# Optimization experiments

Hardware: AMD Instinct MI355X
Metric: run time of the kernel (lower is better)

Reference implementation:

```python
import jax, jax.numpy as jnp
import numpy as np

D_MODEL = 2048
N_HEADS = 32
N_KV_HEADS = 8
HEAD_DIM = D_MODEL // N_HEADS  # 64
THETA = 10000.0
BATCH = 2
SEQ = 2048


def _rope_tables(seq_len, head_dim, theta):
    idx = jnp.arange(0, head_dim, 2, dtype=jnp.float32)
    inv_freq = 1.0 / (theta ** (idx / head_dim))
    pos = jnp.arange(seq_len, dtype=jnp.float32)
    angles = pos[:, None] * inv_freq[None, :]  # (S, head_dim/2)
    return jnp.cos(angles), jnp.sin(angles)


def _apply_rope(x, cos, sin):
    # x: (B, H, S, Dh); cos/sin: (S, Dh/2)
    c = cos[None, None, :, :]
    s = sin[None, None, :, :]
    x_even = x[..., 0::2]
    x_odd = x[..., 1::2]
    out_even = x_even * c - x_odd * s
    out_odd = x_even * s + x_odd * c
    # interleave back: stack on last axis and reshape
    return jnp.stack([out_even, out_odd], axis=-1).reshape(x.shape)


def setup_inputs() -> dict:
    key = jax.random.key(0)
    kx, kq, kk, kv, ko = jax.random.split(key, 5)
    std_sq = (2.0 / (D_MODEL + D_MODEL)) ** 0.5
    std_kv = (2.0 / (D_MODEL + N_KV_HEADS * HEAD_DIM)) ** 0.5
    return {
        "x": jax.random.normal(kx, (BATCH, SEQ, D_MODEL), dtype=jnp.float32),
        "Wq": jax.random.normal(kq, (D_MODEL, D_MODEL), dtype=jnp.float32) * std_sq,
        "Wk": jax.random.normal(kk, (N_KV_HEADS * HEAD_DIM, D_MODEL), dtype=jnp.float32) * std_kv,
        "Wv": jax.random.normal(kv, (N_KV_HEADS * HEAD_DIM, D_MODEL), dtype=jnp.float32) * std_kv,
        "Wo": jax.random.normal(ko, (D_MODEL, D_MODEL), dtype=jnp.float32) * std_sq,
    }


def reference(x, Wq, Wk, Wv, Wo):
    B, S, D = x.shape
    groups = N_HEADS // N_KV_HEADS
    cos, sin = _rope_tables(S, HEAD_DIM, THETA)

    q = (x @ Wq.T).reshape(B, S, N_HEADS, HEAD_DIM).transpose(0, 2, 1, 3)
    k = (x @ Wk.T).reshape(B, S, N_KV_HEADS, HEAD_DIM).transpose(0, 2, 1, 3)
    v = (x @ Wv.T).reshape(B, S, N_KV_HEADS, HEAD_DIM).transpose(0, 2, 1, 3)

    q = _apply_rope(q, cos, sin)
    k = _apply_rope(k, cos, sin)

    # GQA: repeat kv heads (repeat_interleave along head dim)
    k = jnp.repeat(k, groups, axis=1)  # (B, H, S, Dh)
    v = jnp.repeat(v, groups, axis=1)

    scale = 1.0 / jnp.sqrt(jnp.float32(HEAD_DIM))
    scores = jnp.einsum('bhqd,bhkd->bhqk', q, k) * scale
    causal = jnp.tril(jnp.ones((S, S), dtype=bool))
    scores = jnp.where(causal[None, None, :, :], scores, -jnp.inf)
    attn = jax.nn.softmax(scores, axis=-1)
    out = jnp.einsum('bhqk,bhkd->bhqd', attn, v)
    out = out.transpose(0, 2, 1, 3).reshape(B, S, D)
    return out @ Wo.T
```

## Files before the change

### kernel.cpp

```cpp
#include <hip/hip_runtime.h>
#include <math.h>

#define BATCHN 2
#define SEQ 2048
#define DMODEL 2048
#define NH 32
#define NKV 8
#define HDIM 64
#define KVD 512
#define ROWS 4096

typedef __bf16 bf16x8 __attribute__((ext_vector_type(8)));
typedef float f32x4 __attribute__((ext_vector_type(4)));
typedef unsigned short u16x8 __attribute__((ext_vector_type(8)));

#define MFMA(a, b, c) __builtin_amdgcn_mfma_f32_16x16x32_bf16(a, b, c, 0, 0, 0)

__device__ __forceinline__ unsigned short f2bf(float f) {
  union { float f; unsigned u; } v; v.f = f;
  unsigned u = v.u;
  u += 0x7fffu + ((u >> 16) & 1u);
  return (unsigned short)(u >> 16);
}

__device__ __forceinline__ unsigned cvtpk(float a, float b) {
  unsigned r;
  asm("v_cvt_pk_bf16_f32 %0, %1, %2" : "=v"(r) : "v"(a), "v"(b));
  return r;
}
__device__ __forceinline__ void pl32(unsigned& a, unsigned& b) {
  asm("v_permlane32_swap_b32 %0, %1" : "+v"(a), "+v"(b));
}
__device__ __forceinline__ void pl16(unsigned& a, unsigned& b) {
  asm("v_permlane16_swap_b32 %0, %1" : "+v"(a), "+v"(b));
}
__device__ __forceinline__ float exp2v(float x) {
  float r;
  asm("v_exp_f32 %0, %1" : "=v"(r) : "v"(x));
  return r;
}

__device__ __forceinline__ void gload16(const void* g, void* l) {
  __builtin_amdgcn_global_load_lds((const __attribute__((address_space(1))) unsigned int*)g,
                                   (__attribute__((address_space(3))) unsigned int*)l, 16, 0, 0);
}

#define FENCE() asm volatile("" ::: "memory")
#define BARRIER() do { FENCE(); __builtin_amdgcn_s_barrier(); FENCE(); } while (0)
#define LGKM0() asm volatile("s_waitcnt lgkmcnt(0)" ::: "memory")
#define VMCNT(n) asm volatile("s_waitcnt vmcnt(" #n ")" ::: "memory")

__global__ __launch_bounds__(256) void conv_all(const float* __restrict__ x,
                                                const float* __restrict__ Wq,
                                                const float* __restrict__ Wk,
                                                const float* __restrict__ Wv,
                                                const float* __restrict__ Wo,
                                                unsigned short* __restrict__ xb,
                                                unsigned short* __restrict__ Wqb,
                                                unsigned short* __restrict__ Wkb,
                                                unsigned short* __restrict__ Wvb,
                                                unsigned short* __restrict__ Wob,
                                                float* __restrict__ ct,
                                                float* __restrict__ st) {
  int i = blockIdx.x * 256 + threadIdx.x;
  const float* in;
  unsigned short* out;
  int off;
  if (i < 2097152)      { in = x;  out = xb;  off = i; }
  else if (i < 3145728) { in = Wq; out = Wqb; off = i - 2097152; }
  else if (i < 3407872) { in = Wk; out = Wkb; off = i - 3145728; }
  else if (i < 3670016) { in = Wv; out = Wvb; off = i - 3407872; }
  else if (i < 4718592) { in = Wo; out = Wob; off = i - 3670016; }
  else {
    int t = i - 4718592;
    int s = t >> 5, f = t & 31;
    float inv = __expf(-(float)f * (9.210340371976184f / 32.0f));
    float ang = (float)s * inv;
    ct[t] = cosf(ang);
    st[t] = sinf(ang);
    return;
  }
  float4 v = ((const float4*)in)[off];
  ushort4 o;
  o.x = f2bf(v.x); o.y = f2bf(v.y); o.z = f2bf(v.z); o.w = f2bf(v.w);
  ((ushort4*)out)[off] = o;
}

__global__ __launch_bounds__(512, 4) void gemm_qkv8p(const unsigned short* __restrict__ A,
                                                     const unsigned short* __restrict__ Bq,
                                                     const unsigned short* __restrict__ Bk,
                                                     const unsigned short* __restrict__ Bv,
                                                     unsigned short* __restrict__ Qo,
                                                     unsigned short* __restrict__ Ko,
                                                     unsigned short* __restrict__ Vt,
                                                     const float* __restrict__ ct,
                                                     const float* __restrict__ st) {
  __shared__ __align__(16) unsigned short Als[2][128 * 64];
  __shared__ __align__(16) unsigned short Bls[2][128 * 64];
  const int tid = threadIdx.x;
  const int lane = tid & 63, wv = tid >> 6;
  const int wm = wv >> 2, wn = wv & 3;
  const int g = lane >> 4, r15 = lane & 15;
  const int wgid = (blockIdx.x & 7) * 96 + (blockIdx.x >> 3);
  const int bm = wgid / 24, bn = wgid % 24;
  const int row0 = bm << 7;
  const unsigned short* Bp;
  unsigned short* Outb = nullptr;
  int col0, ldo = 0, rope = 0, qsc = 0, isv = 0;
  if (bn < 16)      { Bp = Bq; Outb = Qo; col0 = bn << 7;        ldo = DMODEL; rope = 1; qsc = 1; }
  else if (bn < 20) { Bp = Bk; Outb = Ko; col0 = (bn - 16) << 7; ldo = KVD;    rope = 1; }
  else              { Bp = Bv; col0 = (bn - 20) << 7; isv = 1; }
  const int srow = (wv << 3) + ((lane >> 3) & 7);
  const int scol = (((lane & 7) ^ ((lane >> 3) & 7)) << 3);
  const unsigned short* gA = A + (size_t)(row0 + srow) * DMODEL + scol;
  const unsigned short* gB = Bp + (size_t)(col0 + srow) * DMODEL + scol;
  const int ldsoff = (wv << 9);

  f32x4 acc[4][2];
#pragma unroll
  for (int i = 0; i < 4; ++i) { acc[i][0] = (f32x4){0,0,0,0}; acc[i][1] = (f32x4){0,0,0,0}; }

#define STAGE_A(buf, t, j) gload16(gA + (size_t)((t) * 64) + (size_t)((j) * 64) * DMODEL, \
                                   &Als[buf][(j) * 4096 + ldsoff])
#define STAGE_B(buf, t, j) gload16(gB + (size_t)((t) * 64) + (size_t)((j) * 64) * DMODEL, \
                                   &Bls[buf][(j) * 4096 + ldsoff])
#define RD_A(buf, mf, kk) (*(const bf16x8*)&Als[buf][((wm << 6) + ((mf) << 4) + r15) * 64 + \
                            ((((kk) << 2) + g) ^ (r15 & 7)) * 8])
#define RD_B(buf, nf, kk) (*(const bf16x8*)&Bls[buf][((wn << 5) + ((nf) << 4) + r15) * 64 + \
                            ((((kk) << 2) + g) ^ (r15 & 7)) * 8])

  STAGE_A(0, 0, 0); STAGE_A(0, 0, 1); STAGE_B(0, 0, 0); STAGE_B(0, 0, 1);
  STAGE_A(1, 1, 0); STAGE_A(1, 1, 1); STAGE_B(1, 1, 0); STAGE_B(1, 1, 1);
  VMCNT(4);
  BARRIER();

  const int NT = DMODEL / 64;
  for (int t = 0; t < NT; ++t) {
    const int cur = t & 1;
    bf16x8 bfr[2][2];
#pragma unroll
    for (int nf = 0; nf < 2; ++nf)
#pragma unroll
      for (int kk = 0; kk < 2; ++kk) bfr[nf][kk] = RD_B(cur, nf, kk);
    bf16x8 a00 = RD_A(cur, 0, 0), a01 = RD_A(cur, 0, 1);
    bf16x8 a10 = RD_A(cur, 1, 0), a11 = RD_A(cur, 1, 1);
    if (t >= 1 && t + 1 < NT) { STAGE_A(cur ^ 1, t + 1, 0); STAGE_A(cur ^ 1, t + 1, 1); }
    BARRIER();
    __builtin_amdgcn_s_setprio(1);
#pragma unroll
    for (int nf = 0; nf < 2; ++nf) {
      acc[0][nf] = MFMA(a00, bfr[nf][0], acc[0][nf]);
      acc[0][nf] = MFMA(a01, bfr[nf][1], acc[0][nf]);
      acc[1][nf] = MFMA(a10, bfr[nf][0], acc[1][nf]);
      acc[1][nf] = MFMA(a11, bfr[nf][1], acc[1][nf]);
    }
    __builtin_amdgcn_s_setprio(0);
    BARRIER();
    bf16x8 a20 = RD_A(cur, 2, 0), a21 = RD_A(cur, 2, 1);
    bf16x8 a30 = RD_A(cur, 3, 0), a31 = RD_A(cur, 3, 1);
    if (t + 2 < NT) { STAGE_B(cur, t + 2, 0); STAGE_B(cur, t + 2, 1); }
    BARRIER();
    __builtin_amdgcn_s_setprio(1);
#pragma unroll
    for (int nf = 0; nf < 2; ++nf) {
      acc[2][nf] = MFMA(a20, bfr[nf][0], acc[2][nf]);
      acc[2][nf] = MFMA(a21, bfr[nf][1], acc[2][nf]);
      acc[3][nf] = MFMA(a30, bfr[nf][0], acc[3][nf]);
      acc[3][nf] = MFMA(a31, bfr[nf][1], acc[3][nf]);
    }
    __builtin_amdgcn_s_setprio(0);
    if (t < NT - 1) {
      if (t == NT - 2) VMCNT(0);
      else             VMCNT(2);
    }
    BARRIER();
  }

  if (isv) {
#pragma unroll
    for (int mf = 0; mf < 4; ++mf) {
      const int m0 = row0 + (wm << 6) + (mf << 4) + (g << 2);
      const int b = m0 >> 11, s0 = m0 & (SEQ - 1);
#pragma unroll
      for (int nf = 0; nf < 2; ++nf) {
        const int nv = col0 + (wn << 5) + (nf << 4) + r15;
        ushort4 o;
        o.x = f2bf(acc[mf][nf][0]);
        o.y = f2bf(acc[mf][nf][1]);
        o.z = f2bf(acc[mf][nf][2]);
        o.w = f2bf(acc[mf][nf][3]);
        *(ushort4*)(Vt + ((size_t)(b * NKV * HDIM + nv)) * SEQ + s0) = o;
      }
    }
  } else {
    const float QS = 0.18033688011112042f;
#pragma unroll
    for (int mf = 0; mf < 4; ++mf) {
#pragma unroll
      for (int rr = 0; rr < 4; ++rr) {
        const int m = row0 + (wm << 6) + (mf << 4) + (g << 2) + rr;
        const float* ctr = ct + ((m & (SEQ - 1)) << 5);
        const float* str = st + ((m & (SEQ - 1)) << 5);
#pragma unroll
        for (int nf = 0; nf < 2; ++nf) {
          const int n = col0 + (wn << 5) + (nf << 4) + r15;
          float v = acc[mf][nf][rr];
          float p = __shfl_xor(v, 1);
          if (rope) {
            int fi = (n & 63) >> 1;
            float c = ctr[fi], sn = str[fi];
            v = (lane & 1) ? (p * sn + v * c) : (v * c - p * sn);
          }
          if (qsc) v *= QS;
          Outb[(size_t)m * ldo + n] = f2bf(v);
        }
      }
    }
  }
#undef STAGE_A
#undef STAGE_B
#undef RD_A
#undef RD_B
}

__global__ __launch_bounds__(512) void gemm_out128(const unsigned short* __restrict__ A,
                                                   const unsigned short* __restrict__ B,
                                                   float* __restrict__ C) {
  __shared__ __align__(16) unsigned short Als[3][8192];
  __shared__ __align__(16) unsigned short Bls[3][2][8192];
  const int tid = threadIdx.x, lane = tid & 63, wv = tid >> 6;
  const int wm = wv >> 2, wn = wv & 3;
  const int g = lane >> 4, r15 = lane & 15;
  const int wgid = (blockIdx.x & 7) * 32 + (blockIdx.x >> 3);
  const int bm = wgid >> 3, bn = wgid & 7;
  const int row0 = bm << 7, col0 = bn << 8;
  const int srl = tid >> 3;
  const int sgc = ((tid & 7) ^ (srl & 7)) << 3;
  const unsigned short* gA = A + (size_t)(row0 + srl) * DMODEL + sgc;
  const unsigned short* gB = B + (size_t)(col0 + srl) * DMODEL + sgc;

  f32x4 acc[4][4];
#pragma unroll
  for (int i = 0; i < 4; ++i)
#pragma unroll
    for (int jj = 0; jj < 4; ++jj) acc[i][jj] = (f32x4){0.f, 0.f, 0.f, 0.f};

#define STG_A1(buf, kt) do { \
    gload16(gA + (size_t)(kt) * 64, &Als[buf][(wv << 9)]); \
    gload16(gA + (size_t)64 * DMODEL + (size_t)(kt) * 64, &Als[buf][4096 + (wv << 9)]); } while (0)
#define STG_B1(buf, h, kt) do { \
    gload16(gB + (size_t)((h) * 128) * DMODEL + (kt) * 64, &Bls[buf][h][(wv << 9)]); \
    gload16(gB + (size_t)((h) * 128 + 64) * DMODEL + (kt) * 64, &Bls[buf][h][4096 + (wv << 9)]); } while (0)
#define RA1(buf, mf, kk) (*(const bf16x8*)&Als[buf][((wm << 6) + (mf) * 16 + r15) * 64 + \
                           (((((kk) << 2) + g) ^ (r15 & 7)) << 3)])
#define RB1(buf, nf, kk) (*(const bf16x8*)&Bls[buf][wn >> 1][((wn & 1) * 64 + (nf) * 16 + r15) * 64 + \
                           (((((kk) << 2) + g) ^ (r15 & 7)) << 3)])

  STG_B1(0, 0, 0); STG_B1(0, 1, 0); STG_A1(0, 0);
  STG_B1(1, 0, 1); STG_B1(1, 1, 1); STG_A1(1, 1);
  VMCNT(6);
  BARRIER();

  const int NT = DMODEL / 64;
  for (int t = 0; t < NT; ++t) {
    const int cur = t % 3;
    const int stg = (t + 2) % 3;
    bf16x8 a[4][2], b0[2][2];
#pragma unroll
    for (int mf = 0; mf < 4; ++mf) { a[mf][0] = RA1(cur, mf, 0); a[mf][1] = RA1(cur, mf, 1); }
#pragma unroll
    for (int nf = 0; nf < 2; ++nf) { b0[nf][0] = RB1(cur, nf, 0); b0[nf][1] = RB1(cur, nf, 1); }
    if (t + 2 < NT) { STG_B1(stg, 0, t + 2); STG_B1(stg, 1, t + 2); }
    BARRIER();
    __builtin_amdgcn_s_setprio(1);
#pragma unroll
    for (int mf = 0; mf < 4; ++mf)
#pragma unroll
      for (int nf = 0; nf < 2; ++nf) {
        acc[mf][nf] = MFMA(a[mf][0], b0[nf][0], acc[mf][nf]);
        acc[mf][nf] = MFMA(a[mf][1], b0[nf][1], acc[mf][nf]);
      }
    __builtin_amdgcn_s_setprio(0);
    BARRIER();
    bf16x8 b2[2][2];
#pragma unroll
    for (int nf = 0; nf < 2; ++nf) { b2[nf][0] = RB1(cur, 2 + nf, 0); b2[nf][1] = RB1(cur, 2 + nf, 1); }
    if (t + 2 < NT) STG_A1(stg, t + 2);
    BARRIER();
    __builtin_amdgcn_s_setprio(1);
#pragma unroll
    for (int mf = 0; mf < 4; ++mf)
#pragma unroll
      for (int nf = 0; nf < 2; ++nf) {
        acc[mf][2 + nf] = MFMA(a[mf][0], b2[nf][0], acc[mf][2 + nf]);
        acc[mf][2 + nf] = MFMA(a[mf][1], b2[nf][1], acc[mf][2 + nf]);
      }
    __builtin_amdgcn_s_setprio(0);
    if (t + 2 < NT) { VMCNT(6); }
    else if (t + 2 == NT) { VMCNT(0); }
    BARRIER();
  }
#undef STG_A1
#undef STG_B1
#undef RA1
#undef RB1

#pragma unroll
  for (int mf = 0; mf < 4; ++mf)
#pragma unroll
    for (int rr = 0; rr < 4; ++rr) {
      const int m = row0 + (wm << 6) + (mf) * 16 + (g << 2) + rr;
#pragma unroll
      for (int nf = 0; nf < 4; ++nf)
        C[(size_t)m * DMODEL + col0 + (wn << 6) + (nf << 4) + r15] = acc[mf][nf][rr];
    }
}

__global__ __launch_bounds__(512) void attn_fwd(const unsigned short* __restrict__ Q,
                                                const unsigned short* __restrict__ K,
                                                const unsigned short* __restrict__ Vt,
                                                unsigned short* __restrict__ O) {
  __shared__ __align__(16) unsigned short Kls[2][64 * 64];
  __shared__ __align__(16) unsigned short Vls[2][64 * 64];
  const int bid = blockIdx.x;
  const int xcd = bid & 7;
  const int within = bid >> 3;
  const int grp = xcd * 2 + (within >> 5);
  const int w32 = within & 31;
  const int j = w32 & 7;
  const int hsub = w32 >> 3;
  const int b = grp >> 3, kvh = grp & 7;
  const int h = kvh * 4 + hsub;
  const int wave = threadIdx.x >> 6, lane = threadIdx.x & 63;
  const int g = lane >> 4, r15 = lane & 15;
  const int sr = lane >> 3;
  const int sc = (((lane & 7) << 4) ^ (sr << 4)) >> 1;
  const unsigned short* kbase = K + (size_t)b * SEQ * KVD + kvh * HDIM;
  const unsigned short* vbase = Vt + (size_t)((b * NKV + kvh) * HDIM) * SEQ;

  union { u16x8 s; bf16x8 v; } one8;
#pragma unroll
  for (int z = 0; z < 8; ++z) one8.s[z] = 0x3F80;

  auto STAGE = [&](int bi, int kbv) {
    const int r = wave * 8;
    gload16(kbase + (size_t)(kbv + r + sr) * KVD + sc, &Kls[bi][r * 64]);
    gload16(vbase + (size_t)(r + sr) * SEQ + kbv + sc, &Vls[bi][r * 64]);
  };

#pragma unroll 1
  for (int sel = 0; sel < 2; ++sel) {
    const int qt = sel ? (15 - j) : j;
    const int qrow0 = qt * 128 + wave * 16;
    const unsigned short* qp = Q + (size_t)(b * SEQ + qrow0 + r15) * DMODEL + h * HDIM;
    bf16x8 q0 = *(const bf16x8*)(qp + g * 8);
    bf16x8 q1 = *(const bf16x8*)(qp + 32 + g * 8);
    f32x4 oacc[4] = {};
    f32x4 lacc = {};
    const int kend = (qt + 1) * 128;
    __syncthreads();
    STAGE(0, 0);
    int buf = 0;
    for (int kb = 0; kb < kend; kb += 64) {
      __syncthreads();
      if (kb + 64 < kend) STAGE(buf ^ 1, kb + 64);
      const char* Kc = (const char*)&Kls[buf][0];
      const char* Vc = (const char*)&Vls[buf][0];
      f32x4 s[4];
      __builtin_amdgcn_s_setprio(1);
#pragma unroll
      for (int f = 0; f < 4; ++f) {
        const int r = f * 16 + r15;
        const int sw = (r & 7) << 4;
        bf16x8 k0 = *(const bf16x8*)(Kc + r * 128 + ((g * 16) ^ sw));
        bf16x8 k1 = *(const bf16x8*)(Kc + r * 128 + ((64 + g * 16) ^ sw));
        f32x4 z = {};
        s[f] = MFMA(k1, q1, MFMA(k0, q0, z));
      }
      __builtin_amdgcn_s_setprio(0);
      if (kb + 64 > qrow0) {
        const int q = qrow0 + r15;
#pragma unroll
        for (int f = 0; f < 4; ++f)
#pragma unroll
          for (int rr = 0; rr < 4; ++rr)
            if (kb + f * 16 + g * 4 + rr > q) s[f][rr] = -1e30f;
      }
#pragma unroll
      for (int f = 0; f < 4; ++f)
#pragma unroll
        for (int rr = 0; rr < 4; ++rr) s[f][rr] = exp2v(s[f][rr]);
      bf16x8 p1, p2;
      {
        union { bf16x8 v; unsigned u[4]; } P1, P2;
        unsigned a0 = cvtpk(s[0][0], s[0][1]), b0 = cvtpk(s[1][0], s[1][1]);
        pl32(a0, b0); pl16(a0, b0);
        unsigned a1 = cvtpk(s[0][2], s[0][3]), b1 = cvtpk(s[1][2], s[1][3]);
        pl32(a1, b1); pl16(a1, b1);
        P1.u[0] = a0; P1.u[1] = a1; P1.u[2] = b0; P1.u[3] = b1;
        unsigned a2 = cvtpk(s[2][0], s[2][1]), b2 = cvtpk(s[3][0], s[3][1]);
        pl32(a2, b2); pl16(a2, b2);
        unsigned a3 = cvtpk(s[2][2], s[2][3]), b3 = cvtpk(s[3][2], s[3][3]);
        pl32(a3, b3); pl16(a3, b3);
        P2.u[0] = a2; P2.u[1] = a3; P2.u[2] = b2; P2.u[3] = b3;
        p1 = P1.v; p2 = P2.v;
      }
      lacc = MFMA(p2, one8.v, MFMA(p1, one8.v, lacc));
      __builtin_amdgcn_s_setprio(1);
#pragma unroll
      for (int dc = 0; dc < 4; ++dc) {
        const int r = dc * 16 + r15;
        const int sw = (r & 7) << 4;
        bf16x8 v0 = *(const bf16x8*)(Vc + r * 128 + ((g * 16) ^ sw));
        bf16x8 v1 = *(const bf16x8*)(Vc + r * 128 + ((64 + g * 16) ^ sw));
        oacc[dc] = MFMA(p2, v1, MFMA(p1, v0, oacc[dc]));
      }
      __builtin_amdgcn_s_setprio(0);
      buf ^= 1;
    }
    float rls[4];
#pragma unroll
    for (int rr = 0; rr < 4; ++rr) rls[rr] = 1.0f / lacc[rr];
    unsigned short* optr = O + (size_t)(b * SEQ + qrow0) * DMODEL + h * HDIM;
#pragma unroll
    for (int dc = 0; dc < 4; ++dc)
#pragma unroll
      for (int rr = 0; rr < 4; ++rr)
        optr[(size_t)(g * 4 + rr) * DMODEL + dc * 16 + r15] = f2bf(oacc[dc][rr] * rls[rr]);
  }
}

extern "C" void kernel_launch(void* const* d_in, const int* in_sizes, int n_in,
                              void* d_out, int out_size, void* d_ws, size_t ws_size,
                              hipStream_t stream) {
  const float* x  = (const float*)d_in[0];
  const float* Wq = (const float*)d_in[1];
  const float* Wk = (const float*)d_in[2];
  const float* Wv = (const float*)d_in[3];
  const float* Wo = (const float*)d_in[4];

  char* ws = (char*)d_ws;
  unsigned short* xb  = (unsigned short*)(ws);
  unsigned short* Wqb = (unsigned short*)(ws + (16u << 20));
  unsigned short* Wkb = (unsigned short*)(ws + (24u << 20));
  unsigned short* Wvb = (unsigned short*)(ws + (26u << 20));
  unsigned short* Wob = (unsigned short*)(ws + (28u << 20));
  unsigned short* Qb  = (unsigned short*)(ws + (36u << 20));
  unsigned short* Kb  = (unsigned short*)(ws + (52u << 20));
  unsigned short* Vtb = (unsigned short*)(ws + (60u << 20));
  unsigned short* AO  = (unsigned short*)(ws + (64u << 20));
  float* ct = (float*)(ws + (80u << 20));
  float* st = (float*)(ws + (81u << 20));

  conv_all<<<18688, 256, 0, stream>>>(x, Wq, Wk, Wv, Wo, xb, Wqb, Wkb, Wvb, Wob, ct, st);

  gemm_qkv8p<<<768, 512, 0, stream>>>(xb, Wqb, Wkb, Wvb, Qb, Kb, Vtb, ct, st);

  attn_fwd<<<512, 512, 0, stream>>>(Qb, Kb, Vtb, AO);

  gemm_out128<<<256, 512, 0, stream>>>(AO, Wob, (float*)d_out);
}
```

Measured before the change: 185.4 us.

## Widen QKV GEMM tiles to 128x384 with three B panels per block

The fused QKV projection now has each block compute a 128-row by 384-column tile made of three 128-column weight panels. The grid shrinks from 768 to 256 blocks, exactly one wave on the device's CUs. Each A fragment loaded from LDS feeds three times as many MFMAs, and A traffic from global memory drops threefold. A is triple-buffered and B double-buffered in LDS. The cost is more accumulator registers (launch bounds cut to 2 waves per SIMD), a larger LDS footprint, and a block remap that places blocks sharing rows on the same XCD.

Result: faster. 161.9 us (-12.7%).

```diff
diff --git a/kernel.cpp b/kernel.cpp
--- a/kernel.cpp
+++ b/kernel.cpp
@@ -47,7 +47,6 @@
 
 #define FENCE() asm volatile("" ::: "memory")
 #define BARRIER() do { FENCE(); __builtin_amdgcn_s_barrier(); FENCE(); } while (0)
-#define LGKM0() asm volatile("s_waitcnt lgkmcnt(0)" ::: "memory")
 #define VMCNT(n) asm volatile("s_waitcnt vmcnt(" #n ")" ::: "memory")
 
 __global__ __launch_bounds__(256) void conv_all(const float* __restrict__ x,
@@ -86,141 +85,166 @@
   ((ushort4*)out)[off] = o;
 }
 
-__global__ __launch_bounds__(512, 4) void gemm_qkv8p(const unsigned short* __restrict__ A,
-                                                     const unsigned short* __restrict__ Bq,
-                                                     const unsigned short* __restrict__ Bk,
-                                                     const unsigned short* __restrict__ Bv,
-                                                     unsigned short* __restrict__ Qo,
-                                                     unsigned short* __restrict__ Ko,
-                                                     unsigned short* __restrict__ Vt,
-                                                     const float* __restrict__ ct,
-                                                     const float* __restrict__ st) {
-  __shared__ __align__(16) unsigned short Als[2][128 * 64];
-  __shared__ __align__(16) unsigned short Bls[2][128 * 64];
-  const int tid = threadIdx.x;
-  const int lane = tid & 63, wv = tid >> 6;
+__global__ __launch_bounds__(512, 2) void gemm_qkv384(const unsigned short* __restrict__ A,
+                                                      const unsigned short* __restrict__ Bq,
+                                                      const unsigned short* __restrict__ Bk,
+                                                      const unsigned short* __restrict__ Bv,
+                                                      unsigned short* __restrict__ Qo,
+                                                      unsigned short* __restrict__ Ko,
+                                                      unsigned short* __restrict__ Vt,
+                                                      const float* __restrict__ ct,
+                                                      const float* __restrict__ st) {
+  __shared__ __align__(16) unsigned short Als[3][8192];
+  __shared__ __align__(16) unsigned short Bls[3][2][8192];
+  const int tid = threadIdx.x, lane = tid & 63, wv = tid >> 6;
   const int wm = wv >> 2, wn = wv & 3;
   const int g = lane >> 4, r15 = lane & 15;
-  const int wgid = (blockIdx.x & 7) * 96 + (blockIdx.x >> 3);
-  const int bm = wgid / 24, bn = wgid % 24;
+  const int c = blockIdx.x & 7, i = blockIdx.x >> 3;
+  const int bm = (c >> 1) * 8 + (i & 7);
+  const int grp = (c & 1) * 4 + (i >> 3);
   const int row0 = bm << 7;
-  const unsigned short* Bp;
-  unsigned short* Outb = nullptr;
-  int col0, ldo = 0, rope = 0, qsc = 0, isv = 0;
-  if (bn < 16)      { Bp = Bq; Outb = Qo; col0 = bn << 7;        ldo = DMODEL; rope = 1; qsc = 1; }
-  else if (bn < 20) { Bp = Bk; Outb = Ko; col0 = (bn - 16) << 7; ldo = KVD;    rope = 1; }
-  else              { Bp = Bv; col0 = (bn - 20) << 7; isv = 1; }
-  const int srow = (wv << 3) + ((lane >> 3) & 7);
-  const int scol = (((lane & 7) ^ ((lane >> 3) & 7)) << 3);
+  const unsigned short* Bpan[3];
+  int bnp[3];
+#pragma unroll
+  for (int bk = 0; bk < 3; ++bk) {
+    int p = grp * 3 + bk;
+    bnp[bk] = p;
+    Bpan[bk] = (p < 16) ? Bq + (size_t)(p << 7) * DMODEL
+             : (p < 20) ? Bk + (size_t)((p - 16) << 7) * DMODEL
+                        : Bv + (size_t)((p - 20) << 7) * DMODEL;
+  }
+  const int srow = tid >> 3;
+  const int scol = (((tid & 7) ^ ((tid >> 3) & 7)) << 3);
   const unsigned short* gA = A + (size_t)(row0 + srow) * DMODEL + scol;
-  const unsigned short* gB = Bp + (size_t)(col0 + srow) * DMODEL + scol;
-  const int ldsoff = (wv << 9);
-
-  f32x4 acc[4][2];
-#pragma unroll
-  for (int i = 0; i < 4; ++i) { acc[i][0] = (f32x4){0,0,0,0}; acc[i][1] = (f32x4){0,0,0,0}; }
-
-#define STAGE_A(buf, t, j) gload16(gA + (size_t)((t) * 64) + (size_t)((j) * 64) * DMODEL, \
-                                   &Als[buf][(j) * 4096 + ldsoff])
-#define STAGE_B(buf, t, j) gload16(gB + (size_t)((t) * 64) + (size_t)((j) * 64) * DMODEL, \
-                                   &Bls[buf][(j) * 4096 + ldsoff])
-#define RD_A(buf, mf, kk) (*(const bf16x8*)&Als[buf][((wm << 6) + ((mf) << 4) + r15) * 64 + \
-                            ((((kk) << 2) + g) ^ (r15 & 7)) * 8])
-#define RD_B(buf, nf, kk) (*(const bf16x8*)&Bls[buf][((wn << 5) + ((nf) << 4) + r15) * 64 + \
-                            ((((kk) << 2) + g) ^ (r15 & 7)) * 8])
-
-  STAGE_A(0, 0, 0); STAGE_A(0, 0, 1); STAGE_B(0, 0, 0); STAGE_B(0, 0, 1);
-  STAGE_A(1, 1, 0); STAGE_A(1, 1, 1); STAGE_B(1, 1, 0); STAGE_B(1, 1, 1);
-  VMCNT(4);
+  const unsigned short* gB0 = Bpan[0] + (size_t)srow * DMODEL + scol;
+  const unsigned short* gB1 = Bpan[1] + (size_t)srow * DMODEL + scol;
+  const unsigned short* gB2 = Bpan[2] + (size_t)srow * DMODEL + scol;
+
+  f32x4 acc[4][6];
+#pragma unroll
+  for (int a = 0; a < 4; ++a)
+#pragma unroll
+    for (int b = 0; b < 6; ++b) acc[a][b] = (f32x4){0.f, 0.f, 0.f, 0.f};
+
+#define STG_A(buf, kt) do { \
+    gload16(gA + (size_t)(kt) * 64, &Als[buf][(wv << 9)]); \
+    gload16(gA + (size_t)64 * DMODEL + (size_t)(kt) * 64, &Als[buf][4096 + (wv << 9)]); } while (0)
+#define STG_B(bank, gp, buf, kt) do { \
+    gload16(gp + (size_t)(kt) * 64, &Bls[bank][buf][(wv << 9)]); \
+    gload16(gp + (size_t)64 * DMODEL + (size_t)(kt) * 64, &Bls[bank][buf][4096 + (wv << 9)]); } while (0)
+#define RA(buf, mf, kk) (*(const bf16x8*)&Als[buf][((wm << 6) + ((mf) << 4) + r15) * 64 + \
+                          (((((kk) << 2) + g) ^ (r15 & 7)) << 3)])
+#define RB(bank, buf, sub, kk) (*(const bf16x8*)&Bls[bank][buf][((wn << 5) + ((sub) << 4) + r15) * 64 + \
+                          (((((kk) << 2) + g) ^ (r15 & 7)) << 3)])
+
+  STG_A(0, 0);
+  STG_B(0, gB0, 0, 0); STG_B(1, gB1, 0, 0); STG_B(2, gB2, 0, 0);
+  STG_A(1, 1);
+  VMCNT(0);
   BARRIER();
 
   const int NT = DMODEL / 64;
   for (int t = 0; t < NT; ++t) {
-    const int cur = t & 1;
-    bf16x8 bfr[2][2];
-#pragma unroll
-    for (int nf = 0; nf < 2; ++nf)
-#pragma unroll
-      for (int kk = 0; kk < 2; ++kk) bfr[nf][kk] = RD_B(cur, nf, kk);
-    bf16x8 a00 = RD_A(cur, 0, 0), a01 = RD_A(cur, 0, 1);
-    bf16x8 a10 = RD_A(cur, 1, 0), a11 = RD_A(cur, 1, 1);
-    if (t >= 1 && t + 1 < NT) { STAGE_A(cur ^ 1, t + 1, 0); STAGE_A(cur ^ 1, t + 1, 1); }
+    const int ab = t % 3, an2 = (t + 2) % 3;
+    const int bb = t & 1, bn2 = bb ^ 1;
+    bf16x8 af[4][2];
+#pragma unroll
+    for (int mf = 0; mf < 4; ++mf) { af[mf][0] = RA(ab, mf, 0); af[mf][1] = RA(ab, mf, 1); }
+    bf16x8 b01[2][2][2];
+#pragma unroll
+    for (int bk = 0; bk < 2; ++bk)
+#pragma unroll
+      for (int sub = 0; sub < 2; ++sub) {
+        b01[bk][sub][0] = RB(bk, bb, sub, 0);
+        b01[bk][sub][1] = RB(bk, bb, sub, 1);
+      }
+    if (t + 1 < NT) {
+      STG_B(0, gB0, bn2, t + 1); STG_B(1, gB1, bn2, t + 1); STG_B(2, gB2, bn2, t + 1);
+    }
     BARRIER();
     __builtin_amdgcn_s_setprio(1);
 #pragma unroll
-    for (int nf = 0; nf < 2; ++nf) {
-      acc[0][nf] = MFMA(a00, bfr[nf][0], acc[0][nf]);
-      acc[0][nf] = MFMA(a01, bfr[nf][1], acc[0][nf]);
-      acc[1][nf] = MFMA(a10, bfr[nf][0], acc[1][nf]);
-      acc[1][nf] = MFMA(a11, bfr[nf][1], acc[1][nf]);
+    for (int mf = 0; mf < 4; ++mf)
+#pragma unroll
+      for (int bk = 0; bk < 2; ++bk)
+#pragma unroll
+        for (int sub = 0; sub < 2; ++sub) {
+          acc[mf][bk * 2 + sub] = MFMA(af[mf][0], b01[bk][sub][0], acc[mf][bk * 2 + sub]);
+          acc[mf][bk * 2 + sub] = MFMA(af[mf][1], b01[bk][sub][1], acc[mf][bk * 2 + sub]);
+        }
+    __builtin_amdgcn_s_setprio(0);
+    BARRIER();
+    bf16x8 b2[2][2];
+#pragma unroll
+    for (int sub = 0; sub < 2; ++sub) { b2[sub][0] = RB(2, bb, sub, 0); b2[sub][1] = RB(2, bb, sub, 1); }
+    if (t + 2 < NT) STG_A(an2, t + 2);
+    BARRIER();
+    __builtin_amdgcn_s_setprio(1);
+#pragma unroll
+    for (int mf = 0; mf < 4; ++mf)
+#pragma unroll
+      for (int sub = 0; sub < 2; ++sub) {
+        acc[mf][4 + sub] = MFMA(af[mf][0], b2[sub][0], acc[mf][4 + sub]);
+        acc[mf][4 + sub] = MFMA(af[mf][1], b2[sub][1], acc[mf][4 + sub]);
+      }
+    __builtin_amdgcn_s_setprio(0);
+    if (t + 2 < NT)      { VMCNT(2); }
+    else if (t + 1 < NT) { VMCNT(0); }
+    BARRIER();
+  }
+#undef STG_A
+#undef STG_B
+#undef RA
+#undef RB
+
+  const float QS = 0.18033688011112042f;
+#pragma unroll
+  for (int bk = 0; bk < 3; ++bk) {
+    const int p = bnp[bk];
+    if (p < 20) {
+      unsigned short* Outb = (p < 16) ? Qo : Ko;
+      const int col0 = (p < 16) ? (p << 7) : ((p - 16) << 7);
+      const int ldo = (p < 16) ? DMODEL : KVD;
+      const int qsc = (p < 16);
+#pragma unroll
+      for (int mf = 0; mf < 4; ++mf) {
+#pragma unroll
+        for (int rr = 0; rr < 4; ++rr) {
+          const int m = row0 + (wm << 6) + (mf << 4) + (g << 2) + rr;
+          const float* ctr = ct + ((m & (SEQ - 1)) << 5);
+          const float* str = st + ((m & (SEQ - 1)) << 5);
+#pragma unroll
+          for (int sub = 0; sub < 2; ++sub) {
+            const int n = col0 + (wn << 5) + (sub << 4) + r15;
+            float v = acc[mf][bk * 2 + sub][rr];
+            float pv = __shfl_xor(v, 1);
+            int fi = (n & 63) >> 1;
+            float cc = ctr[fi], sn = str[fi];
+            v = (lane & 1) ? (pv * sn + v * cc) : (v * cc - pv * sn);
+            if (qsc) v *= QS;
+            Outb[(size_t)m * ldo + n] = f2bf(v);
+          }
+        }
+      }
+    } else {
+      const int col0 = (p - 20) << 7;
+#pragma unroll
+      for (int mf = 0; mf < 4; ++mf) {
+        const int m0 = row0 + (wm << 6) + (mf << 4) + (g << 2);
+        const int b = m0 >> 11, s0 = m0 & (SEQ - 1);
+#pragma unroll
+        for (int sub = 0; sub < 2; ++sub) {
+          const int nv = col0 + (wn << 5) + (sub << 4) + r15;
+          ushort4 o;
+          o.x = f2bf(acc[mf][bk * 2 + sub][0]);
+          o.y = f2bf(acc[mf][bk * 2 + sub][1]);
+          o.z = f2bf(acc[mf][bk * 2 + sub][2]);
+          o.w = f2bf(acc[mf][bk * 2 + sub][3]);
+          *(ushort4*)(Vt + ((size_t)(b * NKV * HDIM + nv)) * SEQ + s0) = o;
+        }
+      }
     }
-    __builtin_amdgcn_s_setprio(0);
-    BARRIER();
-    bf16x8 a20 = RD_A(cur, 2, 0), a21 = RD_A(cur, 2, 1);
-    bf16x8 a30 = RD_A(cur, 3, 0), a31 = RD_A(cur, 3, 1);
-    if (t + 2 < NT) { STAGE_B(cur, t + 2, 0); STAGE_B(cur, t + 2, 1); }
-    BARRIER();
-    __builtin_amdgcn_s_setprio(1);
-#pragma unroll
-    for (int nf = 0; nf < 2; ++nf) {
-      acc[2][nf] = MFMA(a20, bfr[nf][0], acc[2][nf]);
-      acc[2][nf] = MFMA(a21, bfr[nf][1], acc[2][nf]);
-      acc[3][nf] = MFMA(a30, bfr[nf][0], acc[3][nf]);
-      acc[3][nf] = MFMA(a31, bfr[nf][1], acc[3][nf]);
-    }
-    __builtin_amdgcn_s_setprio(0);
-    if (t < NT - 1) {
-      if (t == NT - 2) VMCNT(0);
-      else             VMCNT(2);
-    }
-    BARRIER();
-  }
-
-  if (isv) {
-#pragma unroll
-    for (int mf = 0; mf < 4; ++mf) {
-      const int m0 = row0 + (wm << 6) + (mf << 4) + (g << 2);
-      const int b = m0 >> 11, s0 = m0 & (SEQ - 1);
-#pragma unroll
-      for (int nf = 0; nf < 2; ++nf) {
-        const int nv = col0 + (wn << 5) + (nf << 4) + r15;
-        ushort4 o;
-        o.x = f2bf(acc[mf][nf][0]);
-        o.y = f2bf(acc[mf][nf][1]);
-        o.z = f2bf(acc[mf][nf][2]);
-        o.w = f2bf(acc[mf][nf][3]);
-        *(ushort4*)(Vt + ((size_t)(b * NKV * HDIM + nv)) * SEQ + s0) = o;
-      }
-    }
-  } else {
-    const float QS = 0.18033688011112042f;
-#pragma unroll
-    for (int mf = 0; mf < 4; ++mf) {
-#pragma unroll
-      for (int rr = 0; rr < 4; ++rr) {
-        const int m = row0 + (wm << 6) + (mf << 4) + (g << 2) + rr;
-        const float* ctr = ct + ((m & (SEQ - 1)) << 5);
-        const float* str = st + ((m & (SEQ - 1)) << 5);
-#pragma unroll
-        for (int nf = 0; nf < 2; ++nf) {
-          const int n = col0 + (wn << 5) + (nf << 4) + r15;
-          float v = acc[mf][nf][rr];
-          float p = __shfl_xor(v, 1);
-          if (rope) {
-            int fi = (n & 63) >> 1;
-            float c = ctr[fi], sn = str[fi];
-            v = (lane & 1) ? (p * sn + v * c) : (v * c - p * sn);
-          }
-          if (qsc) v *= QS;
-          Outb[(size_t)m * ldo + n] = f2bf(v);
-        }
-      }
-    }
-  }
-#undef STAGE_A
-#undef STAGE_B
-#undef RD_A
-#undef RD_B
+  }
 }
 
 __global__ __launch_bounds__(512) void gemm_out128(const unsigned short* __restrict__ A,
@@ -454,7 +478,7 @@
 
   conv_all<<<18688, 256, 0, stream>>>(x, Wq, Wk, Wv, Wo, xb, Wqb, Wkb, Wvb, Wob, ct, st);
 
-  gemm_qkv8p<<<768, 512, 0, stream>>>(xb, Wqb, Wkb, Wvb, Qb, Kb, Vtb, ct, st);
+  gemm_qkv384<<<256, 512, 0, stream>>>(xb, Wqb, Wkb, Wvb, Qb, Kb, Vtb, ct, st);
 
   attn_fwd<<<512, 512, 0, stream>>>(Qb, Kb, Vtb, AO);
 
```
